# Kernel tuning notes

Hardware: AMD Instinct MI355X
Metric: run time of the kernel (lower is better)

The kernel has to match this reference:

```python
import jax, jax.numpy as jnp
import numpy as np

V = 50000   # vocab_size == output_size
E = 256     # emb_size
H = 512     # hidden_size
B = 128     # batch_size
L = 400     # encoder seq len
T = 100     # decoder history len


def setup_inputs() -> dict:
    key = jax.random.key(0)
    ks = jax.random.split(key, 20)
    s = 0.02
    return {
        "inputs": jax.random.randint(ks[0], (1, B), 0, V),
        "hidden": jax.random.normal(ks[1], (1, B, H), jnp.float32),
        "encoder_hidden": jax.random.normal(ks[2], (L, B, H), jnp.float32),
        "encoder_lengths": jax.random.randint(ks[3], (B,), 0, L),
        "previous_weights": jax.random.normal(ks[4], (B, 1, L), jnp.float32),
        "decoder_hidden": jax.random.normal(ks[5], (T, B, H), jnp.float32),
        "encoder_inputs": jax.random.randint(ks[6], (L, B), 0, V),
        "time_step": 0,
        "emb": jax.random.normal(ks[7], (V, E), jnp.float32) * s,
        "W_ih": jax.random.normal(ks[8], (3 * H, E), jnp.float32) * s,
        "W_hh": jax.random.normal(ks[9], (3 * H, H), jnp.float32) * s,
        "b_ih": jnp.zeros((3 * H,), jnp.float32),
        "b_hh": jnp.zeros((3 * H,), jnp.float32),
        "W_ae": jax.random.normal(ks[10], (H, H), jnp.float32) * s,
        "b_ae": jnp.zeros((H,), jnp.float32),
        "W_ad": jax.random.normal(ks[11], (H, H), jnp.float32) * s,
        "b_ad": jnp.zeros((H,), jnp.float32),
        "W_ptr": jax.random.normal(ks[12], (1, 3 * H), jnp.float32) * s,
        "b_ptr": jnp.zeros((1,), jnp.float32),
        "W_out": jax.random.normal(ks[13], (V, 3 * H), jnp.float32) * s,
        "b_out": jnp.zeros((V,), jnp.float32),
    }


def _gru_step(x, h, W_ih, W_hh, b_ih, b_hh):
    # Single-step torch-style GRU. x: (B,E), h: (B,H)
    hsz = h.shape[-1]
    gi = x @ W_ih.T + b_ih          # (B, 3H)
    gh = h @ W_hh.T + b_hh          # (B, 3H)
    i_r, i_z, i_n = gi[:, :hsz], gi[:, hsz:2 * hsz], gi[:, 2 * hsz:]
    h_r, h_z, h_n = gh[:, :hsz], gh[:, hsz:2 * hsz], gh[:, 2 * hsz:]
    r = jax.nn.sigmoid(i_r + h_r)
    z = jax.nn.sigmoid(i_z + h_z)
    n = jnp.tanh(i_n + r * h_n)
    return (1.0 - z) * n + z * h


def reference(inputs, hidden, encoder_hidden, encoder_lengths, previous_weights,
              decoder_hidden, encoder_inputs, time_step,
              emb, W_ih, W_hh, b_ih, b_hh, W_ae, b_ae, W_ad, b_ad,
              W_ptr, b_ptr, W_out, b_out):
    x = emb[inputs[0]]                       # (B,E)
    h = _gru_step(x, hidden[0], W_ih, W_hh, b_ih, b_hh)   # (B,H) == h_t_d

    enc_len = encoder_hidden.shape[0]
    # encoder attention
    te = h @ W_ae.T + b_ae                   # (B,H)
    e_t = jnp.einsum('bh,lbh->bl', te, encoder_hidden)    # (B,L)
    # faithful reproduction of source mask loop (empty slice -> effectively no-op)
    cond = (enc_len < encoder_lengths)[:, None] & (jnp.arange(enc_len)[None, :] >= encoder_lengths[:, None])
    e_t = jnp.where(cond, -jnp.inf, e_t)
    alpha_e = jax.nn.softmax(e_t, axis=-1)                # (B,L)
    c_t_e = jnp.einsum('bl,lbh->bh', alpha_e, encoder_hidden)

    # decoder (intra) attention
    td = h @ W_ad.T + b_ad
    e_t_d = jnp.einsum('bh,tbh->bt', td, decoder_hidden)  # (B,T)
    alpha_d = jax.nn.softmax(e_t_d, axis=-1)
    c_t_d = jnp.einsum('bt,tbh->bh', alpha_d, decoder_hidden)

    new_hidden = jnp.concatenate([c_t_e, h, c_t_d], axis=-1)   # (B,3H)
    gen = jax.nn.log_softmax(new_hidden @ W_out.T + b_out, axis=-1)  # (B,V)
    pointer_prob = new_hidden @ W_ptr.T + b_ptr                      # (B,1)

    enc_in = encoder_inputs.T                                        # (B,L) int
    alpha_scaled = pointer_prob * alpha_e                            # (B,L)
    vsz = W_out.shape[0]
    bidx = jnp.arange(enc_in.shape[0])[:, None]
    pointer_mask = jnp.zeros((enc_in.shape[0], vsz), gen.dtype).at[bidx, enc_in].add(alpha_scaled)

    final_output = (1.0 - pointer_prob) * gen + pointer_mask         # (B,V)
    return final_output, h[None], previous_weights
```

## Files before the change

kernel.cpp:

```cpp
#include <hip/hip_runtime.h>
#include <cstdint>
#include <cstddef>

#define VV 50000
#define EE 256
#define HH 512
#define BB 128
#define LL 400
#define TT 100
#define H3 1536

struct GemmJob {
    const float* A;
    const float* W;
    const float* bias;
    float*       C;
    int          lda;
    int          K;
};

#define GBN 64
#define GBK 32

__global__ __launch_bounds__(256) void gemm_m128(GemmJob j0, GemmJob j1,
                                                 int N, int ldc)
{
    GemmJob j = (blockIdx.y == 0) ? j0 : j1;
    __shared__ float As[GBK][128];
    __shared__ float Wls[GBK][GBN];

    const int tid = threadIdx.x;
    const int n0  = blockIdx.x * GBN;
    const int tx  = tid & 15;
    const int ty  = tid >> 4;
    const int kq  = tid & 7;
    const int arow = (tid >> 3) * 4;
    const int wrow = (tid >> 3) * 2;

    float acc[8][4];
    #pragma unroll
    for (int i = 0; i < 8; i++)
        #pragma unroll
        for (int jj = 0; jj < 4; jj++) acc[i][jj] = 0.f;

    for (int k0 = 0; k0 < j.K; k0 += GBK) {
        #pragma unroll
        for (int i = 0; i < 4; i++) {
            const float4 v = *(const float4*)(j.A + (size_t)(arow + i) * j.lda + k0 + kq * 4);
            As[kq*4+0][arow+i] = v.x;
            As[kq*4+1][arow+i] = v.y;
            As[kq*4+2][arow+i] = v.z;
            As[kq*4+3][arow+i] = v.w;
        }
        #pragma unroll
        for (int i = 0; i < 2; i++) {
            const int n = n0 + wrow + i;
            float4 v = make_float4(0.f, 0.f, 0.f, 0.f);
            if (n < N) v = *(const float4*)(j.W + (size_t)n * j.K + k0 + kq * 4);
            Wls[kq*4+0][wrow+i] = v.x;
            Wls[kq*4+1][wrow+i] = v.y;
            Wls[kq*4+2][wrow+i] = v.z;
            Wls[kq*4+3][wrow+i] = v.w;
        }
        __syncthreads();
        #pragma unroll
        for (int kk = 0; kk < GBK; kk++) {
            float a[8], w[4];
            #pragma unroll
            for (int i = 0; i < 8; i++) a[i] = As[kk][ty*8+i];
            #pragma unroll
            for (int jj = 0; jj < 4; jj++) w[jj] = Wls[kk][tx*4+jj];
            #pragma unroll
            for (int i = 0; i < 8; i++)
                #pragma unroll
                for (int jj = 0; jj < 4; jj++)
                    acc[i][jj] += a[i] * w[jj];
        }
        __syncthreads();
    }

    const int nbase = n0 + tx * 4;
    #pragma unroll
    for (int i = 0; i < 8; i++) {
        const int b = ty * 8 + i;
        if (nbase + 3 < N) {
            const float4 bb = *(const float4*)(j.bias + nbase);
            float4 r;
            r.x = acc[i][0] + bb.x;
            r.y = acc[i][1] + bb.y;
            r.z = acc[i][2] + bb.z;
            r.w = acc[i][3] + bb.w;
            *(float4*)(j.C + (size_t)b * ldc + nbase) = r;
        } else {
            #pragma unroll
            for (int jj = 0; jj < 4; jj++) {
                const int n = nbase + jj;
                if (n < N) j.C[(size_t)b * ldc + n] = acc[i][jj] + j.bias[n];
            }
        }
    }
}

__global__ __launch_bounds__(256) void gather_emb(const int* __restrict__ tok,
                                                  const float* __restrict__ emb,
                                                  float* __restrict__ x)
{
    const int b = blockIdx.x;
    x[(size_t)b * EE + threadIdx.x] = emb[(size_t)tok[b] * EE + threadIdx.x];
}

__global__ __launch_bounds__(256) void zero_ctx(float* __restrict__ nh)
{
    float* p = nh + (size_t)blockIdx.x * H3;
    const int tid = threadIdx.x;
    p[tid] = 0.f;  p[tid + 256] = 0.f;
    p[1024 + tid] = 0.f;  p[1280 + tid] = 0.f;
}

__global__ __launch_bounds__(256) void gru_combine(const float* __restrict__ gi,
                                                   const float* __restrict__ gh,
                                                   const float* __restrict__ hprev,
                                                   float* __restrict__ nh,
                                                   float* __restrict__ out_h)
{
    const int b = blockIdx.x;
    const int tid = threadIdx.x;
    #pragma unroll
    for (int r = 0; r < 2; r++) {
        const int i = tid + r * 256;
        const size_t base = (size_t)b * H3;
        const float ir = gi[base + i],        hr = gh[base + i];
        const float iz = gi[base + 512 + i],  hz = gh[base + 512 + i];
        const float in_ = gi[base + 1024 + i], hn = gh[base + 1024 + i];
        const float rr = 1.f / (1.f + expf(-(ir + hr)));
        const float zz = 1.f / (1.f + expf(-(iz + hz)));
        const float nn = tanhf(in_ + rr * hn);
        const float hp = hprev[(size_t)b * HH + i];
        const float h  = (1.f - zz) * nn + zz * hp;
        nh[base + 512 + i] = h;
        out_h[(size_t)b * HH + i] = h;
    }
}

__global__ __launch_bounds__(256) void attn_scores(const float* __restrict__ q,
                                                   const float* __restrict__ ctx,
                                                   const int* __restrict__ lens,
                                                   float* __restrict__ out,
                                                   int Lc)
{
    const int b = blockIdx.y;
    const int wave = threadIdx.x >> 6;
    const int lane = threadIdx.x & 63;
    const int l = blockIdx.x * 4 + wave;
    const float* t = q + (size_t)b * HH;
    const float* c = ctx + ((size_t)l * BB + b) * HH;
    float s = 0.f;
    #pragma unroll
    for (int jj = 0; jj < 8; jj++)
        s += t[lane + jj * 64] * c[lane + jj * 64];
    #pragma unroll
    for (int off = 32; off; off >>= 1)
        s += __shfl_down(s, off);
    if (lane == 0) {
        if (lens && (Lc < lens[b]) && (l >= lens[b])) s = -__builtin_inff();
        out[(size_t)b * Lc + l] = s;
    }
}

__global__ __launch_bounds__(256) void softmax2(float* __restrict__ ae, int ne,
                                                float* __restrict__ ad, int nd)
{
    __shared__ float red[256];
    const int tid = threadIdx.x;
    float* row;
    int n;
    if (blockIdx.y == 0) { row = ae + (size_t)blockIdx.x * ne; n = ne; }
    else                 { row = ad + (size_t)blockIdx.x * nd; n = nd; }

    float m = -__builtin_inff();
    for (int i = tid; i < n; i += 256) m = fmaxf(m, row[i]);
    red[tid] = m; __syncthreads();
    for (int s = 128; s; s >>= 1) {
        if (tid < s) red[tid] = fmaxf(red[tid], red[tid + s]);
        __syncthreads();
    }
    m = red[0]; __syncthreads();

    float sum = 0.f;
    for (int i = tid; i < n; i += 256) sum += expf(row[i] - m);
    red[tid] = sum; __syncthreads();
    for (int s = 128; s; s >>= 1) {
        if (tid < s) red[tid] += red[tid + s];
        __syncthreads();
    }
    const float inv = 1.f / red[0];
    for (int i = tid; i < n; i += 256) row[i] = expf(row[i] - m) * inv;
}

__global__ __launch_bounds__(256) void attn_context(const float* __restrict__ alpha,
                                                    const float* __restrict__ ctx,
                                                    float* __restrict__ dst,
                                                    int Lc, int chunk, int off)
{
    __shared__ float al[128];
    const int b = blockIdx.y;
    const int l0 = blockIdx.x * chunk;
    const int tid = threadIdx.x;
    for (int i = tid; i < chunk; i += 256) al[i] = alpha[(size_t)b * Lc + l0 + i];
    __syncthreads();
    float a0 = 0.f, a1 = 0.f;
    for (int ll = 0; ll < chunk; ll++) {
        const float* c = ctx + ((size_t)(l0 + ll) * BB + b) * HH;
        const float w = al[ll];
        a0 += w * c[tid];
        a1 += w * c[tid + 256];
    }
    atomicAdd(&dst[(size_t)b * H3 + off + tid], a0);
    atomicAdd(&dst[(size_t)b * H3 + off + tid + 256], a1);
}

__global__ __launch_bounds__(256) void pointer_kernel(const float* __restrict__ nh,
                                                      const float* __restrict__ W_ptr,
                                                      const float* __restrict__ b_ptr,
                                                      float* __restrict__ pp)
{
    __shared__ float red[256];
    const int b = blockIdx.x;
    const int tid = threadIdx.x;
    float s = 0.f;
    for (int jj = tid; jj < H3; jj += 256) s += nh[(size_t)b * H3 + jj] * W_ptr[jj];
    red[tid] = s; __syncthreads();
    for (int t = 128; t; t >>= 1) {
        if (tid < t) red[tid] += red[tid + t];
        __syncthreads();
    }
    if (tid == 0) pp[b] = red[0] + b_ptr[0];
}

__global__ __launch_bounds__(256) void logsumexp_rows(const float* __restrict__ logits,
                                                      float* __restrict__ lse)
{
    __shared__ float rm[256], rs[256];
    const int b = blockIdx.x;
    const int tid = threadIdx.x;
    const float* row = logits + (size_t)b * VV;
    float m = -__builtin_inff(), s = 0.f;
    for (int i = tid; i < VV; i += 256) {
        const float x = row[i];
        if (x > m) { s = s * expf(m - x) + 1.f; m = x; }
        else       { s += expf(x - m); }
    }
    rm[tid] = m; rs[tid] = s; __syncthreads();
    for (int t = 128; t; t >>= 1) {
        if (tid < t) {
            const float m2 = rm[tid + t], s2 = rs[tid + t];
            const float M = fmaxf(rm[tid], m2);
            rs[tid] = rs[tid] * expf(rm[tid] - M) + s2 * expf(m2 - M);
            rm[tid] = M;
        }
        __syncthreads();
    }
    if (tid == 0) lse[b] = rm[0] + logf(rs[0]);
}

__global__ __launch_bounds__(256) void final_write(float* __restrict__ out,
                                                   const float* __restrict__ pp,
                                                   const float* __restrict__ lse)
{
    const int b = blockIdx.y;
    const int v = (blockIdx.x * 256 + threadIdx.x) * 4;
    if (v >= VV) return;
    float4* p = (float4*)(out + (size_t)b * VV + v);
    float4 x = *p;
    const float g = 1.f - pp[b];
    const float Lse = lse[b];
    x.x = g * (x.x - Lse);
    x.y = g * (x.y - Lse);
    x.z = g * (x.z - Lse);
    x.w = g * (x.w - Lse);
    *p = x;
}

__global__ __launch_bounds__(256) void scatter_pointer(float* __restrict__ out,
                                                       const float* __restrict__ pp,
                                                       const float* __restrict__ alpha_e,
                                                       const int* __restrict__ enc_in)
{
    const int idx = blockIdx.x * 256 + threadIdx.x;
    if (idx >= BB * LL) return;
    const int b = idx / LL;
    const int l = idx - b * LL;
    const int tok = enc_in[(size_t)l * BB + b];
    atomicAdd(&out[(size_t)b * VV + tok], pp[b] * alpha_e[idx]);
}

__global__ __launch_bounds__(256) void copy_pw(float* __restrict__ dst,
                                               const float* __restrict__ src)
{
    const int idx = blockIdx.x * 256 + threadIdx.x;
    if (idx < BB * LL) dst[idx] = src[idx];
}

extern "C" void kernel_launch(void* const* d_in, const int* in_sizes, int n_in,
                              void* d_out, int out_size, void* d_ws, size_t ws_size,
                              hipStream_t stream)
{
    const int*   inputs  = (const int*)  d_in[0];
    const float* hidden  = (const float*)d_in[1];
    const float* enc_h   = (const float*)d_in[2];
    const int*   enc_len = (const int*)  d_in[3];
    const float* prev_w  = (const float*)d_in[4];
    const float* dec_h   = (const float*)d_in[5];
    const int*   enc_in  = (const int*)  d_in[6];
    const float* emb     = (const float*)d_in[8];
    const float* W_ih    = (const float*)d_in[9];
    const float* W_hh    = (const float*)d_in[10];
    const float* b_ih    = (const float*)d_in[11];
    const float* b_hh    = (const float*)d_in[12];
    const float* W_ae    = (const float*)d_in[13];
    const float* b_ae    = (const float*)d_in[14];
    const float* W_ad    = (const float*)d_in[15];
    const float* b_ad    = (const float*)d_in[16];
    const float* W_ptr   = (const float*)d_in[17];
    const float* b_ptr   = (const float*)d_in[18];
    const float* W_out   = (const float*)d_in[19];
    const float* b_out   = (const float*)d_in[20];

    float* out = (float*)d_out;
    float* out_final = out;
    float* out_h     = out + (size_t)BB * VV;
    float* out_pw    = out_h + (size_t)BB * HH;

    float* ws  = (float*)d_ws;
    float* X   = ws;
    float* GI  = X   + BB * EE;
    float* GH  = GI  + BB * H3;
    float* TE  = GH  + BB * H3;
    float* TD  = TE  + BB * HH;
    float* AE  = TD  + BB * HH;
    float* AD  = AE  + BB * LL;
    float* NH  = AD  + BB * TT;
    float* PP  = NH  + BB * H3;
    float* LSE = PP  + BB;

    gather_emb<<<BB, 256, 0, stream>>>(inputs, emb, X);
    zero_ctx<<<BB, 256, 0, stream>>>(NH);

    {
        GemmJob jgi{X,      W_ih, b_ih, GI, EE, EE};
        GemmJob jgh{hidden, W_hh, b_hh, GH, HH, HH};
        gemm_m128<<<dim3(H3 / GBN, 2), 256, 0, stream>>>(jgi, jgh, H3, H3);
    }
    gru_combine<<<BB, 256, 0, stream>>>(GI, GH, hidden, NH, out_h);

    {
        GemmJob jte{NH + 512, W_ae, b_ae, TE, H3, HH};
        GemmJob jtd{NH + 512, W_ad, b_ad, TD, H3, HH};
        gemm_m128<<<dim3(HH / GBN, 2), 256, 0, stream>>>(jte, jtd, HH, HH);
    }

    attn_scores<<<dim3(LL / 4, BB), 256, 0, stream>>>(TE, enc_h, enc_len, AE, LL);
    attn_scores<<<dim3(TT / 4, BB), 256, 0, stream>>>(TD, dec_h, nullptr, AD, TT);

    softmax2<<<dim3(BB, 2), 256, 0, stream>>>(AE, LL, AD, TT);

    attn_context<<<dim3(4, BB), 256, 0, stream>>>(AE, enc_h, NH, LL, 100, 0);
    attn_context<<<dim3(2, BB), 256, 0, stream>>>(AD, dec_h, NH, TT, 50, 1024);

    pointer_kernel<<<BB, 256, 0, stream>>>(NH, W_ptr, b_ptr, PP);

    {
        GemmJob jo{NH, W_out, b_out, out_final, H3, H3};
        gemm_m128<<<dim3((VV + GBN - 1) / GBN, 1), 256, 0, stream>>>(jo, jo, VV, VV);
    }

    logsumexp_rows<<<BB, 256, 0, stream>>>(out_final, LSE);
    final_write<<<dim3((VV / 4 + 255) / 256, BB), 256, 0, stream>>>(out_final, PP, LSE);

    scatter_pointer<<<(BB * LL) / 256, 256, 0, stream>>>(out_final, PP, AE, enc_in);

    copy_pw<<<(BB * LL) / 256, 256, 0, stream>>>(out_pw, prev_w);
}
```

Measured before the change: 1.075 ms.

## Use bf16 MFMA for vocab projection and split logsumexp across chunks

Replaces the fp32 tiled GEMM for the vocabulary projection with a bf16 MFMA kernel. The activations are pre-converted to bf16 and the W_out rows are converted on the fly. The per-row logsumexp is split into ten chunk blocks per row plus a small combine kernel, which raises parallelism. The attention score and context kernels are vectorised and the context work is split into smaller chunks. Rounding to bf16 lowers accuracy of the logits, and the GEMM still streams W_out in fp32 from memory.

Measured after the change: 907.6 us. 1.18x faster.

```diff
diff --git a/kernel.cpp b/kernel.cpp
--- a/kernel.cpp
+++ b/kernel.cpp
@@ -9,6 +9,15 @@
 #define LL 400
 #define TT 100
 #define H3 1536
+
+typedef __attribute__((ext_vector_type(8))) short short8;
+typedef __attribute__((ext_vector_type(4))) float floatx4;
+
+__device__ __forceinline__ unsigned short f2bf(float x) {
+    union { float f; unsigned u; } v; v.f = x;
+    unsigned r = v.u + 0x7fffu + ((v.u >> 16) & 1u);
+    return (unsigned short)(r >> 16);
+}
 
 struct GemmJob {
     const float* A;
@@ -101,6 +110,64 @@
     }
 }
 
+__global__ __launch_bounds__(256) void vocab_mfma(const unsigned short* __restrict__ A,
+                                                  const float* __restrict__ W,
+                                                  const float* __restrict__ bias,
+                                                  float* __restrict__ C)
+{
+    const int wave = threadIdx.x >> 6;
+    const int lane = threadIdx.x & 63;
+    const int quad = lane >> 4;
+    const int nl   = lane & 15;
+    const int n    = blockIdx.x * 64 + wave * 16 + nl;
+    const int nc   = (n < VV) ? n : (VV - 1);
+
+    floatx4 acc[8];
+    #pragma unroll
+    for (int i = 0; i < 8; i++) acc[i] = (floatx4){0.f, 0.f, 0.f, 0.f};
+
+    const float* wp = W + (size_t)nc * H3 + quad * 8;
+    const unsigned short* ap = A + (size_t)nl * H3 + quad * 8;
+
+    for (int k0 = 0; k0 < H3; k0 += 32) {
+        const float4 w0 = *(const float4*)(wp + k0);
+        const float4 w1 = *(const float4*)(wp + k0 + 4);
+        short8 bfrag;
+        bfrag[0] = (short)f2bf(w0.x);
+        bfrag[1] = (short)f2bf(w0.y);
+        bfrag[2] = (short)f2bf(w0.z);
+        bfrag[3] = (short)f2bf(w0.w);
+        bfrag[4] = (short)f2bf(w1.x);
+        bfrag[5] = (short)f2bf(w1.y);
+        bfrag[6] = (short)f2bf(w1.z);
+        bfrag[7] = (short)f2bf(w1.w);
+        #pragma unroll
+        for (int mt = 0; mt < 8; mt++) {
+            const short8 af = *(const short8*)(ap + (size_t)mt * 16 * H3 + k0);
+            acc[mt] = __builtin_amdgcn_mfma_f32_16x16x32_bf16(af, bfrag, acc[mt], 0, 0, 0);
+        }
+    }
+
+    if (n < VV) {
+        const float bv = bias[n];
+        #pragma unroll
+        for (int mt = 0; mt < 8; mt++) {
+            #pragma unroll
+            for (int r = 0; r < 4; r++) {
+                const int m = mt * 16 + quad * 4 + r;
+                C[(size_t)m * VV + n] = acc[mt][r] + bv;
+            }
+        }
+    }
+}
+
+__global__ __launch_bounds__(256) void nh_to_bf16(const float* __restrict__ nh,
+                                                  unsigned short* __restrict__ out)
+{
+    const int idx = blockIdx.x * 256 + threadIdx.x;
+    out[idx] = f2bf(nh[idx]);
+}
+
 __global__ __launch_bounds__(256) void gather_emb(const int* __restrict__ tok,
                                                   const float* __restrict__ emb,
                                                   float* __restrict__ x)
@@ -152,12 +219,12 @@
     const int wave = threadIdx.x >> 6;
     const int lane = threadIdx.x & 63;
     const int l = blockIdx.x * 4 + wave;
-    const float* t = q + (size_t)b * HH;
-    const float* c = ctx + ((size_t)l * BB + b) * HH;
-    float s = 0.f;
-    #pragma unroll
-    for (int jj = 0; jj < 8; jj++)
-        s += t[lane + jj * 64] * c[lane + jj * 64];
+    const float4* q4 = (const float4*)(q + (size_t)b * HH);
+    const float4* c4 = (const float4*)(ctx + ((size_t)l * BB + b) * HH);
+    const float4 a0 = q4[lane],      b0 = c4[lane];
+    const float4 a1 = q4[lane + 64], b1 = c4[lane + 64];
+    float s = a0.x*b0.x + a0.y*b0.y + a0.z*b0.z + a0.w*b0.w
+            + a1.x*b1.x + a1.y*b1.y + a1.z*b1.z + a1.w*b1.w;
     #pragma unroll
     for (int off = 32; off; off >>= 1)
         s += __shfl_down(s, off);
@@ -202,21 +269,22 @@
                                                     float* __restrict__ dst,
                                                     int Lc, int chunk, int off)
 {
-    __shared__ float al[128];
+    __shared__ float al[32];
     const int b = blockIdx.y;
     const int l0 = blockIdx.x * chunk;
     const int tid = threadIdx.x;
-    for (int i = tid; i < chunk; i += 256) al[i] = alpha[(size_t)b * Lc + l0 + i];
+    if (tid < chunk) al[tid] = alpha[(size_t)b * Lc + l0 + tid];
     __syncthreads();
-    float a0 = 0.f, a1 = 0.f;
+    float ax = 0.f, ay = 0.f;
     for (int ll = 0; ll < chunk; ll++) {
-        const float* c = ctx + ((size_t)(l0 + ll) * BB + b) * HH;
+        const float2* c = (const float2*)(ctx + ((size_t)(l0 + ll) * BB + b) * HH);
+        const float2 v = c[tid];
         const float w = al[ll];
-        a0 += w * c[tid];
-        a1 += w * c[tid + 256];
-    }
-    atomicAdd(&dst[(size_t)b * H3 + off + tid], a0);
-    atomicAdd(&dst[(size_t)b * H3 + off + tid + 256], a1);
+        ax += w * v.x;
+        ay += w * v.y;
+    }
+    atomicAdd(&dst[(size_t)b * H3 + off + tid * 2 + 0], ax);
+    atomicAdd(&dst[(size_t)b * H3 + off + tid * 2 + 1], ay);
 }
 
 __global__ __launch_bounds__(256) void pointer_kernel(const float* __restrict__ nh,
@@ -237,20 +305,25 @@
     if (tid == 0) pp[b] = red[0] + b_ptr[0];
 }
 
-__global__ __launch_bounds__(256) void logsumexp_rows(const float* __restrict__ logits,
-                                                      float* __restrict__ lse)
+#define LSE_CHUNKS 10
+#define LSE_SPAN 5000
+
+__global__ __launch_bounds__(256) void lse_part(const float* __restrict__ logits,
+                                                float2* __restrict__ part)
 {
     __shared__ float rm[256], rs[256];
-    const int b = blockIdx.x;
-    const int tid = threadIdx.x;
-    const float* row = logits + (size_t)b * VV;
-    float m = -__builtin_inff(), s = 0.f;
-    for (int i = tid; i < VV; i += 256) {
-        const float x = row[i];
-        if (x > m) { s = s * expf(m - x) + 1.f; m = x; }
-        else       { s += expf(x - m); }
-    }
-    rm[tid] = m; rs[tid] = s; __syncthreads();
+    const int b = blockIdx.y;
+    const int s = blockIdx.x;
+    const int tid = threadIdx.x;
+    const float4* row = (const float4*)(logits + (size_t)b * VV + (size_t)s * LSE_SPAN);
+    float m = -__builtin_inff(), sum = 0.f;
+    for (int i = tid; i < LSE_SPAN / 4; i += 256) {
+        const float4 v = row[i];
+        const float mx = fmaxf(fmaxf(v.x, v.y), fmaxf(v.z, v.w));
+        if (mx > m) { sum *= expf(m - mx); m = mx; }
+        sum += expf(v.x - m) + expf(v.y - m) + expf(v.z - m) + expf(v.w - m);
+    }
+    rm[tid] = m; rs[tid] = sum; __syncthreads();
     for (int t = 128; t; t >>= 1) {
         if (tid < t) {
             const float m2 = rm[tid + t], s2 = rs[tid + t];
@@ -260,7 +333,22 @@
         }
         __syncthreads();
     }
-    if (tid == 0) lse[b] = rm[0] + logf(rs[0]);
+    if (tid == 0) part[(size_t)b * LSE_CHUNKS + s] = make_float2(rm[0], rs[0]);
+}
+
+__global__ __launch_bounds__(128) void lse_final(const float2* __restrict__ part,
+                                                 float* __restrict__ lse)
+{
+    const int b = threadIdx.x;
+    float m = -__builtin_inff(), s = 0.f;
+    #pragma unroll
+    for (int i = 0; i < LSE_CHUNKS; i++) {
+        const float2 p = part[(size_t)b * LSE_CHUNKS + i];
+        const float M = fmaxf(m, p.x);
+        s = s * expf(m - M) + p.y * expf(p.x - M);
+        m = M;
+    }
+    lse[b] = m + logf(s);
 }
 
 __global__ __launch_bounds__(256) void final_write(float* __restrict__ out,
@@ -342,6 +430,8 @@
     float* NH  = AD  + BB * TT;
     float* PP  = NH  + BB * H3;
     float* LSE = PP  + BB;
+    float2* PART = (float2*)(LSE + BB);
+    unsigned short* ABF = (unsigned short*)(PART + BB * LSE_CHUNKS);
 
     gather_emb<<<BB, 256, 0, stream>>>(inputs, emb, X);
     zero_ctx<<<BB, 256, 0, stream>>>(NH);
@@ -364,17 +454,16 @@
 
     softmax2<<<dim3(BB, 2), 256, 0, stream>>>(AE, LL, AD, TT);
 
-    attn_context<<<dim3(4, BB), 256, 0, stream>>>(AE, enc_h, NH, LL, 100, 0);
-    attn_context<<<dim3(2, BB), 256, 0, stream>>>(AD, dec_h, NH, TT, 50, 1024);
+    attn_context<<<dim3(LL / 25, BB), 256, 0, stream>>>(AE, enc_h, NH, LL, 25, 0);
+    attn_context<<<dim3(TT / 25, BB), 256, 0, stream>>>(AD, dec_h, NH, TT, 25, 1024);
 
     pointer_kernel<<<BB, 256, 0, stream>>>(NH, W_ptr, b_ptr, PP);
 
-    {
-        GemmJob jo{NH, W_out, b_out, out_final, H3, H3};
-        gemm_m128<<<dim3((VV + GBN - 1) / GBN, 1), 256, 0, stream>>>(jo, jo, VV, VV);
-    }
-
-    logsumexp_rows<<<BB, 256, 0, stream>>>(out_final, LSE);
+    nh_to_bf16<<<(BB * H3) / 256, 256, 0, stream>>>(NH, ABF);
+    vocab_mfma<<<(VV + 63) / 64, 256, 0, stream>>>(ABF, W_out, b_out, out_final);
+
+    lse_part<<<dim3(LSE_CHUNKS, BB), 256, 0, stream>>>(out_final, PART);
+    lse_final<<<1, 128, 0, stream>>>(PART, LSE);
     final_write<<<dim3((VV / 4 + 255) / 256, BB), 256, 0, stream>>>(out_final, PP, LSE);
 
     scatter_pointer<<<(BB * LL) / 256, 256, 0, stream>>>(out_final, PP, AE, enc_in);
```
